# Performance work log

Hardware: AMD Instinct MI355X
Metric: run time of the kernel (lower is better)

Reference implementation:

```python
import jax, jax.numpy as jnp
import numpy as np

B = 262144
HIST = 24
FORE = 20
HID = 256
# torch: tau_int = clamp(tau,1,18).long().item(); default tau=6.0 -> static 6 (host sync in torch)
TAU_INT = 6


def setup_inputs() -> dict:
    key = jax.random.key(0)
    ks = jax.random.split(key, 9)
    s = 0.1
    return {
        "history": jax.random.normal(ks[0], (B, HIST), jnp.float32),
        "enc_w1": jax.random.normal(ks[1], (HIST + FORE, HID), jnp.float32) * s,
        "enc_b1": jnp.zeros((HID,), jnp.float32),
        "enc_w2": jax.random.normal(ks[2], (HID, HID), jnp.float32) * s,
        "enc_b2": jnp.zeros((HID,), jnp.float32),
        "cor_w1": jax.random.normal(ks[3], (HID, HID), jnp.float32) * s,
        "cor_b1": jnp.zeros((HID,), jnp.float32),
        "cor_w2": jax.random.normal(ks[4], (HID, FORE), jnp.float32) * s,
        "cor_b2": jnp.zeros((FORE,), jnp.float32),
        "alpha": jnp.float32(0.2),
        "beta": jnp.float32(0.3),
        "gamma": jnp.float32(0.01),
        "tau": jnp.float32(6.0),
        "lambda_mix": jnp.float32(0.5),
    }


def _physics_core(history, alpha, beta, gamma, steps):
    a = jax.nn.sigmoid(alpha)
    b = jax.nn.sigmoid(beta)
    g = jnp.abs(gamma)
    T0 = history[:, -1]                      # [B]
    buf0 = history[:, -TAU_INT:].T           # [tau, B]; buf0[0] = history[:, -tau]

    def step(carry, _):
        T, buf = carry
        T_delayed = buf[0]
        T_new = T - a * T - b * T_delayed - g * T ** 3
        buf = jnp.concatenate([buf[1:], T_new[None, :]], axis=0)
        return (T_new, buf), T_new

    _, preds = jax.lax.scan(step, (T0, buf0), None, length=steps)
    return preds.T                            # [B, steps]


def reference(history, enc_w1, enc_b1, enc_w2, enc_b2,
              cor_w1, cor_b1, cor_w2, cor_b2,
              alpha, beta, gamma, tau, lambda_mix):
    T_physics = _physics_core(history, alpha, beta, gamma, FORE)   # [B, FORE]
    combined = jnp.concatenate([history, T_physics], axis=1)       # [B, HIST+FORE]
    h = jnp.tanh(combined @ enc_w1 + enc_b1)
    features = jnp.tanh(h @ enc_w2 + enc_b2)
    c = jnp.tanh(features @ cor_w1 + cor_b1)
    T_soft = c @ cor_w2 + cor_b2                                   # [B, FORE]
    lam = jax.nn.sigmoid(lambda_mix)
    T_pred = T_physics + lam * T_soft
    return (T_pred, T_physics, T_soft)
```

## Files before the change

### kernel.cpp

```cpp
#include <hip/hip_runtime.h>
#include <hip/hip_bf16.h>

#define NROWS 262144
#define HISTC 24
#define FOREC 20

typedef __bf16        v8bf __attribute__((ext_vector_type(8)));
typedef float         v4f  __attribute__((ext_vector_type(4)));
typedef float         v2f  __attribute__((ext_vector_type(2)));
typedef unsigned int  v4u  __attribute__((ext_vector_type(4)));
typedef unsigned int  v2u  __attribute__((ext_vector_type(2)));

#define WS_WT1_OFF 64
#define WT1_ELEMS 16384
#define WT2_ELEMS 65536
#define WT3_ELEMS 65536
#define WT4R_ELEMS 65536

#define TANH_C 2.885390081777927f

__device__ __forceinline__ unsigned short f2bf(float x) {
    unsigned u = __builtin_bit_cast(unsigned, x);
    u += 0x7FFFu + ((u >> 16) & 1u);
    return (unsigned short)(u >> 16);
}

__device__ __forceinline__ unsigned packbf2(float a, float b) {
    unsigned ua = __builtin_bit_cast(unsigned, a) + 0x8000u;
    unsigned ub = __builtin_bit_cast(unsigned, b) + 0x8000u;
    return __builtin_amdgcn_perm(ub, ua, 0x07060302u);
}

__device__ __forceinline__ void lds_barrier() {
    asm volatile("s_waitcnt lgkmcnt(0)\n\ts_barrier" ::: "memory");
}

__device__ __forceinline__ int swzi(int r, int byteoff) {
    return (r << 8) + (((byteoff) ^ ((r & 7) << 4)) >> 1);
}

__global__ void prep_kernel(const float* __restrict__ w1, const float* __restrict__ w2,
                            const float* __restrict__ w3, const float* __restrict__ w4,
                            const float* __restrict__ alpha, const float* __restrict__ beta,
                            const float* __restrict__ gamma, const float* __restrict__ lmix,
                            unsigned char* __restrict__ ws)
{
    if (blockIdx.x == 104) {
        int t = threadIdx.x;
        float* wsf = (float*)ws;
        if (t == 0) wsf[0] = 1.0f / (1.0f + expf(-alpha[0]));
        else if (t == 1) wsf[1] = 1.0f / (1.0f + expf(-beta[0]));
        else if (t == 2) wsf[2] = fabsf(gamma[0]);
        else if (t == 3) wsf[3] = 1.0f / (1.0f + expf(-lmix[0]));
        return;
    }
    int idx = (blockIdx.x * 256 + threadIdx.x) * 8;
    const float* src;
    int KT, Kreal, Nreal, srcN, local, ntmask;
    unsigned short* dst = (unsigned short*)(ws + WS_WT1_OFF);
    if (idx < WT1_ELEMS) {
        local = idx; src = w1; KT = 2; Kreal = 44; Nreal = 256; srcN = 256; ntmask = 255;
    } else if (idx < WT1_ELEMS + WT2_ELEMS) {
        local = idx - WT1_ELEMS; dst += WT1_ELEMS;
        src = w2; KT = 8; Kreal = 256; Nreal = 256; srcN = 256; ntmask = 255;
    } else if (idx < WT1_ELEMS + WT2_ELEMS + WT3_ELEMS) {
        local = idx - (WT1_ELEMS + WT2_ELEMS); dst += WT1_ELEMS + WT2_ELEMS;
        src = w3; KT = 8; Kreal = 256; Nreal = 256; srcN = 256; ntmask = 255;
    } else {
        local = idx - (WT1_ELEMS + WT2_ELEMS + WT3_ELEMS);
        dst += WT1_ELEMS + WT2_ELEMS + WT3_ELEMS;
        src = w4; KT = 8; Kreal = 256; Nreal = 20; srcN = 20; ntmask = 1;
    }
    int L   = (local >> 3) & 63;
    int blk = local >> 9;
    int kt = blk % KT, nt = (blk / KT) & ntmask;
    int cc = L & 15,  qq = L >> 4;
    int feat = nt * 16 + cc;
    int kbase = kt * 32 + qq * 8;
    unsigned short tmp[8];
#pragma unroll
    for (int j = 0; j < 8; ++j) {
        int k = kbase + j;
        float v = (k < Kreal && feat < Nreal) ? src[k * srcN + feat] : 0.0f;
        tmp[j] = f2bf(v);
    }
    v4u pk;
    pk[0] = tmp[0] | ((unsigned)tmp[1] << 16);
    pk[1] = tmp[2] | ((unsigned)tmp[3] << 16);
    pk[2] = tmp[4] | ((unsigned)tmp[5] << 16);
    pk[3] = tmp[6] | ((unsigned)tmp[7] << 16);
    *(v4u*)&dst[local] = pk;
}

template<int KT, int KTN, int S0>
__device__ __forceinline__ void layer_pipe(const char* bin, char* bout,
        const v4u* __restrict__ wp, const v4u* __restrict__ wpn,
        const float* __restrict__ bias, v4u A[3][4],
        const int* be, const int* bo, const int* wb, const int* fx,
        int w, int q, int lane)
{
    v4f acc[4][4];
#pragma unroll
    for (int ft = 0; ft < 4; ++ft)
#pragma unroll
        for (int st = 0; st < 4; ++st) {
            v4f z = {0.0f, 0.0f, 0.0f, 0.0f};
            acc[ft][st] = z;
        }

    v4u Bf[2][4];
#pragma unroll
    for (int st = 0; st < 4; ++st)
        Bf[0][st] = *(const v4u*)(bin + be[st]);

#pragma unroll
    for (int kt = 0; kt < KT; ++kt) {
        const int cs = (S0 + kt) % 3;
        const int ps = (S0 + kt + 2) % 3;
        if (kt + 2 < KT) {
#pragma unroll
            for (int ft = 0; ft < 4; ++ft)
                A[ps][ft] = wp[((w * 4 + ft) * KT + kt + 2) * 64 + lane];
        } else {
#pragma unroll
            for (int ft = 0; ft < 4; ++ft)
                A[ps][ft] = wpn[((w * 4 + ft) * KTN + (kt + 2 - KT)) * 64 + lane];
        }
        if (kt + 1 < KT) {
            const int kn = kt + 1;
#pragma unroll
            for (int st = 0; st < 4; ++st)
                Bf[kn & 1][st] = *(const v4u*)(bin + ((kn & 1) ? bo[st] : be[st]) + kn * 64);
        }
        __builtin_amdgcn_s_setprio(1);
#pragma unroll
        for (int st = 0; st < 4; ++st) {
            v8bf bb = __builtin_bit_cast(v8bf, Bf[kt & 1][st]);
#pragma unroll
            for (int ft = 0; ft < 4; ++ft)
                acc[ft][st] = __builtin_amdgcn_mfma_f32_16x16x32_bf16(
                    __builtin_bit_cast(v8bf, A[cs][ft]), bb, acc[ft][st], 0, 0, 0);
        }
        __builtin_amdgcn_s_setprio(0);
    }


    const v2f C2   = {TANH_C, TANH_C};
    const v2f one2 = {1.0f, 1.0f};
    const v2f m22  = {-2.0f, -2.0f};
#pragma unroll
    for (int ft = 0; ft < 4; ++ft) {
        v4f bi = *(const v4f*)&bias[w * 64 + ft * 16 + q * 4];
        v2f bi01 = {bi[0], bi[1]}, bi23 = {bi[2], bi[3]};
        v2f bic01 = bi01 * C2, bic23 = bi23 * C2;
#pragma unroll
        for (int st = 0; st < 4; ++st) {
            v4f a = acc[ft][st];
            v2f a01 = {a[0], a[1]}, a23 = {a[2], a[3]};
            v2f t01 = __builtin_elementwise_fma(a01, C2, bic01);
            v2f t23 = __builtin_elementwise_fma(a23, C2, bic23);
            v2f p01, p23;
            p01[0] = __builtin_amdgcn_exp2f(t01[0]);
            p01[1] = __builtin_amdgcn_exp2f(t01[1]);
            p23[0] = __builtin_amdgcn_exp2f(t23[0]);
            p23[1] = __builtin_amdgcn_exp2f(t23[1]);
            v2f d01 = p01 + one2;
            v2f d23 = p23 + one2;
            v2f rc01, rc23;
            rc01[0] = __builtin_amdgcn_rcpf(d01[0]);
            rc01[1] = __builtin_amdgcn_rcpf(d01[1]);
            rc23[0] = __builtin_amdgcn_rcpf(d23[0]);
            rc23[1] = __builtin_amdgcn_rcpf(d23[1]);
            v2f x01 = __builtin_elementwise_fma(rc01, m22, one2);
            v2f x23 = __builtin_elementwise_fma(rc23, m22, one2);
            v2u d; d[0] = packbf2(x01[0], x01[1]); d[1] = packbf2(x23[0], x23[1]);
            *(v2u*)(bout + wb[st] + fx[ft]) = d;
        }
    }
    lds_barrier();
}

__global__ __launch_bounds__(256, 2) void fused_kernel(
    const float* __restrict__ history,
    const float* __restrict__ eb1, const float* __restrict__ eb2,
    const float* __restrict__ cb1, const float* __restrict__ cb2,
    const unsigned char* __restrict__ ws, float* __restrict__ out)
{
    __shared__ unsigned short buf[2][64 * 256];
    __shared__ float tp[64 * 20];
    char* b0 = (char*)&buf[0][0];
    char* b1 = (char*)&buf[1][0];

    const int tid  = threadIdx.x;
    const int w    = tid >> 6;
    const int lane = tid & 63;
    const int c    = lane & 15;
    const int q    = lane >> 4;
    const int row0 = blockIdx.x << 6;
    const float* wsf = (const float*)ws;
    const v4u* wp1 = (const v4u*)(ws + WS_WT1_OFF);
    const v4u* wp2 = wp1 + WT1_ELEMS / 8;
    const v4u* wp3 = wp2 + WT2_ELEMS / 8;
    const v4u* wp4 = wp3 + WT3_ELEMS / 8;

    const int e    = (c >> 2) & 1;
    const int d64  = e << 6;
    const int qp_r = (q * 16) ^ ((c & 3) << 4);
    int be[4], bo[4], wb[4], fx[4];
#pragma unroll
    for (int st = 0; st < 4; ++st) {
        int br = (st * 16 + c) * 512 + qp_r;
        be[st] = br + d64;
        bo[st] = br - d64;
        wb[st] = (st * 16 + c) * 512 + w * 128 + ((q * 8) ^ ((c & 1) << 4));
    }
#pragma unroll
    for (int ft = 0; ft < 4; ++ft)
        fx[ft] = (ft * 32) ^ (((c >> 1) & 3) << 5);

    v4u A[3][4];
#pragma unroll
    for (int ft = 0; ft < 4; ++ft) {
        A[0][ft] = wp1[((w * 4 + ft) * 2 + 0) * 64 + lane];
        A[1][ft] = wp1[((w * 4 + ft) * 2 + 1) * 64 + lane];
    }

#pragma unroll
    for (int i = 0; i < 2; ++i) {
        int e2 = tid + i * 256;
        if (e2 < 384) {
            int r  = e2 / 6, c4 = e2 - r * 6;
            v4f h4 = *(const v4f*)&history[(long)(row0 + r) * 24 + c4 * 4];
            v2u d; d[0] = packbf2(h4[0], h4[1]); d[1] = packbf2(h4[2], h4[3]);
            *(v2u*)&buf[0][swzi(r, c4 * 8)] = d;
        }
    }
#pragma unroll
    for (int i = 0; i < 2; ++i) {
        int e2 = tid + i * 256;
        if (e2 < 320) {
            int r = e2 / 5, g = e2 - r * 5;
            v2u z = {0u, 0u};
            *(v2u*)&buf[0][swzi(r, 88 + g * 8)] = z;
        }
    }
    if (tid < 64) {
        const float* hrow = &history[(long)(row0 + tid) * 24];
        v2f h18 = *(const v2f*)&hrow[18];
        v4f h20 = *(const v4f*)&hrow[20];
        float pa = wsf[0], pb = wsf[1], pg = wsf[2];
        float d0 = h18[0], d1 = h18[1], d2 = h20[0];
        float d3 = h20[1], d4 = h20[2], d5 = h20[3];
        float T = d5;
#pragma unroll
        for (int s = 0; s < 20; ++s) {
            float t3 = T * T * T;
            float Tn = T - pa * T;
            Tn = Tn - pb * d0;
            Tn = Tn - pg * t3;
            tp[tid * 20 + s] = Tn;
            buf[0][swzi(tid, 48 + 2 * s)] = f2bf(Tn);
            d0 = d1; d1 = d2; d2 = d3; d3 = d4; d4 = d5; d5 = Tn;
            T = Tn;
        }
    }
    lds_barrier();

    layer_pipe<2, 8, 0>(b0, b1, wp1, wp2, eb1, A, be, bo, wb, fx, w, q, lane);
    layer_pipe<8, 8, 2>(b1, b0, wp2, wp3, eb2, A, be, bo, wb, fx, w, q, lane);
    layer_pipe<8, 8, 1>(b0, b1, wp3, wp4, cb1, A, be, bo, wb, fx, w, q, lane);

    const int b04 = (w * 16 + c) * 512 + qp_r;
    v4f acc40 = {0.0f, 0.0f, 0.0f, 0.0f}, acc41 = {0.0f, 0.0f, 0.0f, 0.0f};
    v4u bcur = *(const v4u*)(b1 + b04 + d64);
#pragma unroll
    for (int kt = 0; kt < 8; ++kt) {
        const int cs = kt % 3, ps = (kt + 2) % 3;
        if (kt + 2 < 8) {
            A[ps][0] = wp4[((w * 4 + 0) * 8 + kt + 2) * 64 + lane];
            A[ps][1] = wp4[((w * 4 + 1) * 8 + kt + 2) * 64 + lane];
        }
        v4u bnext;
        if (kt + 1 < 8)
            bnext = *(const v4u*)(b1 + b04 + (((kt + 1) & 1) ? -d64 : d64) + (kt + 1) * 64);
        acc40 = __builtin_amdgcn_mfma_f32_16x16x32_bf16(
            __builtin_bit_cast(v8bf, A[cs][0]), __builtin_bit_cast(v8bf, bcur), acc40, 0, 0, 0);
        acc41 = __builtin_amdgcn_mfma_f32_16x16x32_bf16(
            __builtin_bit_cast(v8bf, A[cs][1]), __builtin_bit_cast(v8bf, bcur), acc41, 0, 0, 0);
        if (kt + 1 < 8) bcur = bnext;
    }

    const float lam = wsf[3];
    const long sample = (long)row0 + w * 16 + c;
    float* outP = out;
    float* outF = out + (long)NROWS * 20;
    float* outS = out + (long)NROWS * 40;
    {
        int f0 = q * 4;
        v4f bi  = *(const v4f*)&cb2[f0];
        v4f tph = *(const v4f*)&tp[(w * 16 + c) * 20 + f0];
        v4f ts, pr;
#pragma unroll
        for (int r = 0; r < 4; ++r) {
            ts[r] = acc40[r] + bi[r];
            pr[r] = tph[r] + lam * ts[r];
        }
        *(v4f*)&outS[sample * 20 + f0] = ts;
        *(v4f*)&outP[sample * 20 + f0] = pr;
        *(v4f*)&outF[sample * 20 + f0] = tph;
    }
    if (q == 0) {
        v4f bi  = *(const v4f*)&cb2[16];
        v4f tph = *(const v4f*)&tp[(w * 16 + c) * 20 + 16];
        v4f ts, pr;
#pragma unroll
        for (int r = 0; r < 4; ++r) {
            ts[r] = acc41[r] + bi[r];
            pr[r] = tph[r] + lam * ts[r];
        }
        *(v4f*)&outS[sample * 20 + 16] = ts;
        *(v4f*)&outP[sample * 20 + 16] = pr;
        *(v4f*)&outF[sample * 20 + 16] = tph;
    }
}

extern "C" void kernel_launch(void* const* d_in, const int* in_sizes, int n_in,
                              void* d_out, int out_size, void* d_ws, size_t ws_size,
                              hipStream_t stream)
{
    const float* history = (const float*)d_in[0];
    const float* enc_w1  = (const float*)d_in[1];
    const float* enc_b1  = (const float*)d_in[2];
    const float* enc_w2  = (const float*)d_in[3];
    const float* enc_b2  = (const float*)d_in[4];
    const float* cor_w1  = (const float*)d_in[5];
    const float* cor_b1  = (const float*)d_in[6];
    const float* cor_w2  = (const float*)d_in[7];
    const float* cor_b2  = (const float*)d_in[8];
    const float* alpha   = (const float*)d_in[9];
    const float* beta    = (const float*)d_in[10];
    const float* gamma   = (const float*)d_in[11];
    const float* lmix    = (const float*)d_in[13];

    prep_kernel<<<105, 256, 0, stream>>>(enc_w1, enc_w2, cor_w1, cor_w2,
                                         alpha, beta, gamma, lmix,
                                         (unsigned char*)d_ws);
    fused_kernel<<<NROWS / 64, 256, 0, stream>>>(history, enc_b1, enc_b2, cor_b1, cor_b2,
                                                 (const unsigned char*)d_ws, (float*)d_out);
}
```

Baseline: 202.0 us.

## Process 128 rows per block with single in-place LDS activation buffer

Each block now handles 128 samples instead of 64, so every weight fragment loaded from global memory feeds twice as many MFMAs. Activations live in one in-place LDS buffer instead of ping-pong buffers, with an extra barrier between the matmul phase and the tanh writeback. Total LDS use stays about the same. The weight-prefetch pipeline drops from three stages to two, and the accumulator count doubles to 32 vectors per thread, which raises register pressure and may lower occupancy or cause spills.

```diff
diff --git a/kernel.cpp b/kernel.cpp
--- a/kernel.cpp
+++ b/kernel.cpp
@@ -4,6 +4,7 @@
 #define NROWS 262144
 #define HISTC 24
 #define FOREC 20
+#define BROWS 128
 
 typedef __bf16        v8bf __attribute__((ext_vector_type(8)));
 typedef float         v4f  __attribute__((ext_vector_type(4)));
@@ -92,58 +93,75 @@
     *(v4u*)&dst[local] = pk;
 }
 
-template<int KT, int KTN, int S0>
-__device__ __forceinline__ void layer_pipe(const char* bin, char* bout,
+template<int KT, int KTN>
+__device__ __forceinline__ void layer_pipe(char* bufc,
         const v4u* __restrict__ wp, const v4u* __restrict__ wpn,
-        const float* __restrict__ bias, v4u A[3][4],
-        const int* be, const int* bo, const int* wb, const int* fx,
+        const float* __restrict__ bias, v4u A[2][4],
+        int be0, int bo0, const int* wfx,
         int w, int q, int lane)
 {
-    v4f acc[4][4];
+    v4f acc[4][8];
 #pragma unroll
     for (int ft = 0; ft < 4; ++ft)
 #pragma unroll
-        for (int st = 0; st < 4; ++st) {
+        for (int st = 0; st < 8; ++st) {
             v4f z = {0.0f, 0.0f, 0.0f, 0.0f};
             acc[ft][st] = z;
         }
 
     v4u Bf[2][4];
 #pragma unroll
-    for (int st = 0; st < 4; ++st)
-        Bf[0][st] = *(const v4u*)(bin + be[st]);
+    for (int j = 0; j < 4; ++j)
+        Bf[0][j] = *(const v4u*)(bufc + be0 + j * 8192);
 
 #pragma unroll
     for (int kt = 0; kt < KT; ++kt) {
-        const int cs = (S0 + kt) % 3;
-        const int ps = (S0 + kt + 2) % 3;
-        if (kt + 2 < KT) {
+        const int cs = kt & 1;
+        const int ps = cs ^ 1;
+        if (kt + 1 < KT) {
 #pragma unroll
             for (int ft = 0; ft < 4; ++ft)
-                A[ps][ft] = wp[((w * 4 + ft) * KT + kt + 2) * 64 + lane];
+                A[ps][ft] = wp[((w * 4 + ft) * KT + kt + 1) * 64 + lane];
         } else {
 #pragma unroll
             for (int ft = 0; ft < 4; ++ft)
-                A[ps][ft] = wpn[((w * 4 + ft) * KTN + (kt + 2 - KT)) * 64 + lane];
-        }
+                A[ps][ft] = wpn[((w * 4 + ft) * KTN + 0) * 64 + lane];
+        }
+        {
+            const int rb = cs ? bo0 : be0;
+#pragma unroll
+            for (int j = 0; j < 4; ++j)
+                Bf[1][j] = *(const v4u*)(bufc + rb + (4 + j) * 8192 + kt * 64);
+        }
+        __builtin_amdgcn_s_setprio(1);
+#pragma unroll
+        for (int j = 0; j < 4; ++j) {
+            v8bf bb = __builtin_bit_cast(v8bf, Bf[0][j]);
+#pragma unroll
+            for (int ft = 0; ft < 4; ++ft)
+                acc[ft][j] = __builtin_amdgcn_mfma_f32_16x16x32_bf16(
+                    __builtin_bit_cast(v8bf, A[cs][ft]), bb, acc[ft][j], 0, 0, 0);
+        }
+        __builtin_amdgcn_s_setprio(0);
         if (kt + 1 < KT) {
-            const int kn = kt + 1;
-#pragma unroll
-            for (int st = 0; st < 4; ++st)
-                Bf[kn & 1][st] = *(const v4u*)(bin + ((kn & 1) ? bo[st] : be[st]) + kn * 64);
+            const int rb = ps ? bo0 : be0;
+#pragma unroll
+            for (int j = 0; j < 4; ++j)
+                Bf[0][j] = *(const v4u*)(bufc + rb + j * 8192 + (kt + 1) * 64);
         }
         __builtin_amdgcn_s_setprio(1);
 #pragma unroll
-        for (int st = 0; st < 4; ++st) {
-            v8bf bb = __builtin_bit_cast(v8bf, Bf[kt & 1][st]);
+        for (int j = 0; j < 4; ++j) {
+            v8bf bb = __builtin_bit_cast(v8bf, Bf[1][j]);
 #pragma unroll
             for (int ft = 0; ft < 4; ++ft)
-                acc[ft][st] = __builtin_amdgcn_mfma_f32_16x16x32_bf16(
-                    __builtin_bit_cast(v8bf, A[cs][ft]), bb, acc[ft][st], 0, 0, 0);
+                acc[ft][4 + j] = __builtin_amdgcn_mfma_f32_16x16x32_bf16(
+                    __builtin_bit_cast(v8bf, A[cs][ft]), bb, acc[ft][4 + j], 0, 0, 0);
         }
         __builtin_amdgcn_s_setprio(0);
     }
 
+    lds_barrier();
 
     const v2f C2   = {TANH_C, TANH_C};
     const v2f one2 = {1.0f, 1.0f};
@@ -154,7 +172,7 @@
         v2f bi01 = {bi[0], bi[1]}, bi23 = {bi[2], bi[3]};
         v2f bic01 = bi01 * C2, bic23 = bi23 * C2;
 #pragma unroll
-        for (int st = 0; st < 4; ++st) {
+        for (int st = 0; st < 8; ++st) {
             v4f a = acc[ft][st];
             v2f a01 = {a[0], a[1]}, a23 = {a[2], a[3]};
             v2f t01 = __builtin_elementwise_fma(a01, C2, bic01);
@@ -174,7 +192,7 @@
             v2f x01 = __builtin_elementwise_fma(rc01, m22, one2);
             v2f x23 = __builtin_elementwise_fma(rc23, m22, one2);
             v2u d; d[0] = packbf2(x01[0], x01[1]); d[1] = packbf2(x23[0], x23[1]);
-            *(v2u*)(bout + wb[st] + fx[ft]) = d;
+            *(v2u*)(bufc + wfx[ft] + st * 8192) = d;
         }
     }
     lds_barrier();
@@ -186,17 +204,16 @@
     const float* __restrict__ cb1, const float* __restrict__ cb2,
     const unsigned char* __restrict__ ws, float* __restrict__ out)
 {
-    __shared__ unsigned short buf[2][64 * 256];
-    __shared__ float tp[64 * 20];
-    char* b0 = (char*)&buf[0][0];
-    char* b1 = (char*)&buf[1][0];
+    __shared__ unsigned short buf[BROWS * 256];
+    __shared__ float tp[BROWS * 20];
+    char* bufc = (char*)buf;
 
     const int tid  = threadIdx.x;
     const int w    = tid >> 6;
     const int lane = tid & 63;
     const int c    = lane & 15;
     const int q    = lane >> 4;
-    const int row0 = blockIdx.x << 6;
+    const int row0 = blockIdx.x << 7;
     const float* wsf = (const float*)ws;
     const v4u* wp1 = (const v4u*)(ws + WS_WT1_OFF);
     const v4u* wp2 = wp1 + WT1_ELEMS / 8;
@@ -206,45 +223,36 @@
     const int e    = (c >> 2) & 1;
     const int d64  = e << 6;
     const int qp_r = (q * 16) ^ ((c & 3) << 4);
-    int be[4], bo[4], wb[4], fx[4];
-#pragma unroll
-    for (int st = 0; st < 4; ++st) {
-        int br = (st * 16 + c) * 512 + qp_r;
-        be[st] = br + d64;
-        bo[st] = br - d64;
-        wb[st] = (st * 16 + c) * 512 + w * 128 + ((q * 8) ^ ((c & 1) << 4));
-    }
+    const int be0  = c * 512 + qp_r + d64;
+    const int bo0  = c * 512 + qp_r - d64;
+    int wfx[4];
 #pragma unroll
     for (int ft = 0; ft < 4; ++ft)
-        fx[ft] = (ft * 32) ^ (((c >> 1) & 3) << 5);
-
-    v4u A[3][4];
-#pragma unroll
-    for (int ft = 0; ft < 4; ++ft) {
+        wfx[ft] = c * 512 + w * 128 + ((ft * 32 + q * 8) ^ ((c & 7) << 4));
+
+    v4u A[2][4];
+#pragma unroll
+    for (int ft = 0; ft < 4; ++ft)
         A[0][ft] = wp1[((w * 4 + ft) * 2 + 0) * 64 + lane];
-        A[1][ft] = wp1[((w * 4 + ft) * 2 + 1) * 64 + lane];
-    }
-
-#pragma unroll
-    for (int i = 0; i < 2; ++i) {
+
+#pragma unroll
+    for (int i = 0; i < 3; ++i) {
         int e2 = tid + i * 256;
-        if (e2 < 384) {
-            int r  = e2 / 6, c4 = e2 - r * 6;
-            v4f h4 = *(const v4f*)&history[(long)(row0 + r) * 24 + c4 * 4];
-            v2u d; d[0] = packbf2(h4[0], h4[1]); d[1] = packbf2(h4[2], h4[3]);
-            *(v2u*)&buf[0][swzi(r, c4 * 8)] = d;
-        }
-    }
-#pragma unroll
-    for (int i = 0; i < 2; ++i) {
+        int r  = e2 / 6, c4 = e2 - r * 6;
+        v4f h4 = *(const v4f*)&history[(long)(row0 + r) * 24 + c4 * 4];
+        v2u d; d[0] = packbf2(h4[0], h4[1]); d[1] = packbf2(h4[2], h4[3]);
+        *(v2u*)&buf[swzi(r, c4 * 8)] = d;
+    }
+#pragma unroll
+    for (int i = 0; i < 3; ++i) {
         int e2 = tid + i * 256;
-        if (e2 < 320) {
+        if (e2 < 640) {
             int r = e2 / 5, g = e2 - r * 5;
             v2u z = {0u, 0u};
-            *(v2u*)&buf[0][swzi(r, 88 + g * 8)] = z;
-        }
-    }
-    if (tid < 64) {
+            *(v2u*)&buf[swzi(r, 88 + g * 8)] = z;
+        }
+    }
+    if (tid < BROWS) {
         const float* hrow = &history[(long)(row0 + tid) * 24];
         v2f h18 = *(const v2f*)&hrow[18];
         v4f h20 = *(const v4f*)&hrow[20];
@@ -259,68 +267,87 @@
             Tn = Tn - pb * d0;
             Tn = Tn - pg * t3;
             tp[tid * 20 + s] = Tn;
-            buf[0][swzi(tid, 48 + 2 * s)] = f2bf(Tn);
+            buf[swzi(tid, 48 + 2 * s)] = f2bf(Tn);
             d0 = d1; d1 = d2; d2 = d3; d3 = d4; d4 = d5; d5 = Tn;
             T = Tn;
         }
     }
     lds_barrier();
 
-    layer_pipe<2, 8, 0>(b0, b1, wp1, wp2, eb1, A, be, bo, wb, fx, w, q, lane);
-    layer_pipe<8, 8, 2>(b1, b0, wp2, wp3, eb2, A, be, bo, wb, fx, w, q, lane);
-    layer_pipe<8, 8, 1>(b0, b1, wp3, wp4, cb1, A, be, bo, wb, fx, w, q, lane);
-
-    const int b04 = (w * 16 + c) * 512 + qp_r;
-    v4f acc40 = {0.0f, 0.0f, 0.0f, 0.0f}, acc41 = {0.0f, 0.0f, 0.0f, 0.0f};
-    v4u bcur = *(const v4u*)(b1 + b04 + d64);
+    layer_pipe<2, 8>(bufc, wp1, wp2, eb1, A, be0, bo0, wfx, w, q, lane);
+    layer_pipe<8, 8>(bufc, wp2, wp3, eb2, A, be0, bo0, wfx, w, q, lane);
+    layer_pipe<8, 8>(bufc, wp3, wp4, cb1, A, be0, bo0, wfx, w, q, lane);
+
+    const int b4e = be0 + w * 16384;
+    const int b4o = bo0 + w * 16384;
+    v4f a4[2][2];
+#pragma unroll
+    for (int s2 = 0; s2 < 2; ++s2)
+#pragma unroll
+        for (int ft = 0; ft < 2; ++ft) {
+            v4f z = {0.0f, 0.0f, 0.0f, 0.0f};
+            a4[s2][ft] = z;
+        }
+    v4u Aw[2][2];
+    Aw[0][0] = A[0][0]; Aw[0][1] = A[0][1];
+    v4u B4[2][2];
+    B4[0][0] = *(const v4u*)(bufc + b4e);
+    B4[0][1] = *(const v4u*)(bufc + b4e + 8192);
 #pragma unroll
     for (int kt = 0; kt < 8; ++kt) {
-        const int cs = kt % 3, ps = (kt + 2) % 3;
-        if (kt + 2 < 8) {
-            A[ps][0] = wp4[((w * 4 + 0) * 8 + kt + 2) * 64 + lane];
-            A[ps][1] = wp4[((w * 4 + 1) * 8 + kt + 2) * 64 + lane];
-        }
-        v4u bnext;
-        if (kt + 1 < 8)
-            bnext = *(const v4u*)(b1 + b04 + (((kt + 1) & 1) ? -d64 : d64) + (kt + 1) * 64);
-        acc40 = __builtin_amdgcn_mfma_f32_16x16x32_bf16(
-            __builtin_bit_cast(v8bf, A[cs][0]), __builtin_bit_cast(v8bf, bcur), acc40, 0, 0, 0);
-        acc41 = __builtin_amdgcn_mfma_f32_16x16x32_bf16(
-            __builtin_bit_cast(v8bf, A[cs][1]), __builtin_bit_cast(v8bf, bcur), acc41, 0, 0, 0);
-        if (kt + 1 < 8) bcur = bnext;
+        const int cs = kt & 1, ps = cs ^ 1;
+        if (kt + 1 < 8) {
+            Aw[ps][0] = wp4[((w * 4 + 0) * 8 + kt + 1) * 64 + lane];
+            Aw[ps][1] = wp4[((w * 4 + 1) * 8 + kt + 1) * 64 + lane];
+            const int rb = ps ? b4o : b4e;
+            B4[ps][0] = *(const v4u*)(bufc + rb + (kt + 1) * 64);
+            B4[ps][1] = *(const v4u*)(bufc + rb + 8192 + (kt + 1) * 64);
+        }
+#pragma unroll
+        for (int s2 = 0; s2 < 2; ++s2) {
+            v8bf bb = __builtin_bit_cast(v8bf, B4[cs][s2]);
+#pragma unroll
+            for (int ft = 0; ft < 2; ++ft)
+                a4[s2][ft] = __builtin_amdgcn_mfma_f32_16x16x32_bf16(
+                    __builtin_bit_cast(v8bf, Aw[cs][ft]), bb, a4[s2][ft], 0, 0, 0);
+        }
     }
 
     const float lam = wsf[3];
-    const long sample = (long)row0 + w * 16 + c;
     float* outP = out;
     float* outF = out + (long)NROWS * 20;
     float* outS = out + (long)NROWS * 40;
-    {
-        int f0 = q * 4;
-        v4f bi  = *(const v4f*)&cb2[f0];
-        v4f tph = *(const v4f*)&tp[(w * 16 + c) * 20 + f0];
-        v4f ts, pr;
-#pragma unroll
-        for (int r = 0; r < 4; ++r) {
-            ts[r] = acc40[r] + bi[r];
-            pr[r] = tph[r] + lam * ts[r];
-        }
-        *(v4f*)&outS[sample * 20 + f0] = ts;
-        *(v4f*)&outP[sample * 20 + f0] = pr;
-        *(v4f*)&outF[sample * 20 + f0] = tph;
-    }
-    if (q == 0) {
-        v4f bi  = *(const v4f*)&cb2[16];
-        v4f tph = *(const v4f*)&tp[(w * 16 + c) * 20 + 16];
-        v4f ts, pr;
-#pragma unroll
-        for (int r = 0; r < 4; ++r) {
-            ts[r] = acc41[r] + bi[r];
-            pr[r] = tph[r] + lam * ts[r];
-        }
-        *(v4f*)&outS[sample * 20 + 16] = ts;
-        *(v4f*)&outP[sample * 20 + 16] = pr;
-        *(v4f*)&outF[sample * 20 + 16] = tph;
+#pragma unroll
+    for (int s2 = 0; s2 < 2; ++s2) {
+        const int trow = (w * 2 + s2) * 16 + c;
+        const long sample = (long)row0 + trow;
+        {
+            int f0 = q * 4;
+            v4f bi  = *(const v4f*)&cb2[f0];
+            v4f tph = *(const v4f*)&tp[trow * 20 + f0];
+            v4f ts, pr;
+#pragma unroll
+            for (int r = 0; r < 4; ++r) {
+                ts[r] = a4[s2][0][r] + bi[r];
+                pr[r] = tph[r] + lam * ts[r];
+            }
+            *(v4f*)&outS[sample * 20 + f0] = ts;
+            *(v4f*)&outP[sample * 20 + f0] = pr;
+            *(v4f*)&outF[sample * 20 + f0] = tph;
+        }
+        if (q == 0) {
+            v4f bi  = *(const v4f*)&cb2[16];
+            v4f tph = *(const v4f*)&tp[trow * 20 + 16];
+            v4f ts, pr;
+#pragma unroll
+            for (int r = 0; r < 4; ++r) {
+                ts[r] = a4[s2][1][r] + bi[r];
+                pr[r] = tph[r] + lam * ts[r];
+            }
+            *(v4f*)&outS[sample * 20 + 16] = ts;
+            *(v4f*)&outP[sample * 20 + 16] = pr;
+            *(v4f*)&outF[sample * 20 + 16] = tph;
+        }
     }
 }
 
@@ -345,6 +372,8 @@
     prep_kernel<<<105, 256, 0, stream>>>(enc_w1, enc_w2, cor_w1, cor_w2,
                                          alpha, beta, gamma, lmix,
                                          (unsigned char*)d_ws);
-    fused_kernel<<<NROWS / 64, 256, 0, stream>>>(history, enc_b1, enc_b2, cor_b1, cor_b2,
-                                                 (const unsigned char*)d_ws, (float*)d_out);
-}
+    fused_kernel<<<NROWS / BROWS, 256, 0, stream>>>(history, enc_b1, enc_b2,
+                                                    cor_b1, cor_b2,
+                                                    (const unsigned char*)d_ws,
+                                                    (float*)d_out);
+}
```

Result: no change. 201.0 us (-0.5%).
